# Kernel tuning notes

Hardware: AMD Instinct MI355X
Metric: run time of the kernel (lower is better)

The kernel has to match this reference:

```python
import jax, jax.numpy as jnp
import numpy as np

FORGET_BIAS = 1.0  # tf LSTMCell default

def _lstm_step(c, h, xt, W, b):
    # tf LSTMCell: gates = [x, h] @ W + b, split order (i, j, f, o)
    gates = jnp.concatenate([xt, h], axis=-1) @ W + b
    i, j, f, o = jnp.split(gates, 4, axis=-1)
    c_new = c * jax.nn.sigmoid(f + FORGET_BIAS) + jax.nn.sigmoid(i) * jnp.tanh(j)
    h_new = jnp.tanh(c_new) * jax.nn.sigmoid(o)
    return c_new, h_new

def setup_inputs() -> dict:
    key = jax.random.key(0)
    k1, k2, k3 = jax.random.split(key, 3)
    B, T, H = 512, 1024, 64
    x = jax.random.normal(k1, (B, T, 1), dtype=jnp.float32)
    W1 = jax.random.normal(k2, (1 + H, 4 * H), dtype=jnp.float32) * 0.1
    b1 = jnp.zeros((4 * H,), dtype=jnp.float32)
    W2 = jax.random.normal(k3, (H + 1, 4 * 1), dtype=jnp.float32) * 0.1
    b2 = jnp.zeros((4,), dtype=jnp.float32)
    return {"x": x, "W1": W1, "b1": b1, "W2": W2, "b2": b2}

def reference(x, W1, b1, W2, b2):
    B, T, _ = x.shape
    H = W1.shape[1] // 4
    xs = jnp.swapaxes(x, 0, 1)  # [T, B, 1]

    def step(carry, xt):
        c1, h1, c2, h2 = carry
        c1, h1 = _lstm_step(c1, h1, xt, W1, b1)   # layer 1: in=1, hidden=64
        c2, h2 = _lstm_step(c2, h2, h1, W2, b2)   # layer 2: in=64, hidden=1
        return (c1, h1, c2, h2), h2

    init = (jnp.zeros((B, H), x.dtype), jnp.zeros((B, H), x.dtype),
            jnp.zeros((B, 1), x.dtype), jnp.zeros((B, 1), x.dtype))
    _, ys = jax.lax.scan(step, init, xs)  # ys: [T, B, 1]
    return jnp.swapaxes(ys, 0, 1)  # [B, T, 1]
```

## Files before the change

kernel.cpp:

```cpp
#include <hip/hip_runtime.h>


#define TT 1024

__device__ __forceinline__ float fsig(float x) {
    return __builtin_amdgcn_rcpf(1.f + __expf(-x));
}
__device__ __forceinline__ float ftanh(float x) {
    return 1.f - 2.f * __builtin_amdgcn_rcpf(1.f + __expf(2.f * x));
}

template <int Ctrl, int Rmask>
__device__ __forceinline__ float dpp_add(float x) {
    int t = __builtin_amdgcn_update_dpp(0, __float_as_int(x), Ctrl, Rmask, 0xf, true);
    return x + __int_as_float(t);
}
__device__ __forceinline__ float wave_sum64(float x) {
    x = dpp_add<0x111, 0xf>(x);
    x = dpp_add<0x112, 0xf>(x);
    x = dpp_add<0x114, 0xf>(x);
    x = dpp_add<0x118, 0xf>(x);
    x = dpp_add<0x142, 0xa>(x);
    x = dpp_add<0x143, 0xc>(x);
    return x;
}

__global__ __launch_bounds__(576, 6) void lstm2_kernel(
    const float* __restrict__ x,
    const float* __restrict__ W1,
    const float* __restrict__ b1,
    const float* __restrict__ W2,
    const float* __restrict__ b2,
    float* __restrict__ y)
{
    __shared__ __align__(16) float xs[TT];
    __shared__ __align__(16) float h1s[2][64];
    __shared__ __align__(16) float gs[2][64][4];

    const int tid  = threadIdx.x;
    const int b    = blockIdx.x;
    const int lane = tid & 63;
    const int cw   = tid >> 6;
    const int half = lane >> 5;
    const int l31  = lane & 31;

    if (tid < 256) {
        ((float4*)xs)[tid] = ((const float4*)(x + (size_t)b * TT))[tid];
    }
    if (tid < 128) ((float*)h1s)[tid] = 0.f;

    float* yrow = y + (size_t)b * TT;

    if (cw < 8) {
        const int col   = (cw << 5) | l31;
        const int g     = cw >> 1;
        const int gunit = ((cw & 1) << 5) | l31;

        float w[33];
        float bias = 0.f;
        if (half == 0) {
            w[0] = W1[col];
            bias = b1[col];
#pragma unroll
            for (int j = 1; j <= 32; ++j) w[j] = W1[j * 256 + col];
        } else {
            w[0] = 0.f;
#pragma unroll
            for (int j = 1; j <= 32; ++j) w[j] = W1[(32 + j) * 256 + col];
        }

        const float L2E = 1.4426950408889634f;
        const float mm = (g == 1) ? 2.f * L2E : -L2E;
        const float kk = (g == 2) ? -L2E : 0.f;
        const float aa = (g == 1) ? 1.f : 0.f;
        const float bb = (g == 1) ? -2.f : 1.f;

        const int hrow = half << 3;
        float c1 = 0.f;
        __syncthreads();

#define STEP(PAR, XT) { \
        float a0 = fmaf((XT), w[0], bias), a1 = 0.f, a2 = 0.f, a3 = 0.f; \
        const float4* hb = (const float4*)(&h1s[(PAR) ^ 1][0]); \
        _Pragma("unroll") \
        for (int q = 0; q < 8; ++q) { \
            float4 h4 = hb[hrow + q]; \
            a0 = fmaf(h4.x, w[1 + 4 * q], a0); \
            a1 = fmaf(h4.y, w[2 + 4 * q], a1); \
            a2 = fmaf(h4.z, w[3 + 4 * q], a2); \
            a3 = fmaf(h4.w, w[4 + 4 * q], a3); \
        } \
        float p = (a0 + a1) + (a2 + a3); \
        p += __shfl_xor(p, 32); \
        float act = fmaf(bb, __builtin_amdgcn_rcpf(1.f + exp2f(fmaf(mm, p, kk))), aa); \
        gs[PAR][gunit][g] = act; \
        __syncthreads(); \
        float4 g4 = *(const float4*)(&gs[PAR][lane][0]); \
        c1 = fmaf(c1, g4.z, g4.x * g4.y); \
        float rr = __builtin_amdgcn_rcpf(1.f + exp2f(c1 * (2.f * L2E))); \
        float tt_ = rr * g4.w; \
        h1s[PAR][lane] = fmaf(-2.f, tt_, g4.w); }

        for (int t = 0; t < TT; t += 4) {
            float4 x4 = *(const float4*)(xs + t);
            STEP(0, x4.x)
            STEP(1, x4.y)
            STEP(0, x4.z)
            STEP(1, x4.w)
        }
#undef STEP
        __syncthreads();
    } else {
        float4 w2g4 = *(const float4*)(W2 + lane * 4);
        const float w2h0 = W2[256], w2h1 = W2[257], w2h2 = W2[258], w2h3 = W2[259];
        const float b20 = b2[0], b21 = b2[1], b22 = b2[2], b23 = b2[3];
        float c2 = 0.f, h2 = 0.f;
        __syncthreads();

        for (int t = 0; t < TT; ++t) {
            __syncthreads();
            if (t > 0) {
                const float hv = h1s[(t - 1) & 1][lane];
                const float d0 = wave_sum64(hv * w2g4.x);
                const float d1 = wave_sum64(hv * w2g4.y);
                const float d2 = wave_sum64(hv * w2g4.z);
                const float d3 = wave_sum64(hv * w2g4.w);
                if (lane == 63) {
                    const float i2 = fsig (fmaf(h2, w2h0, d0) + b20);
                    const float j2 = ftanh(fmaf(h2, w2h1, d1) + b21);
                    const float f2 = fsig (fmaf(h2, w2h2, d2) + b22 + 1.f);
                    const float o2 = fsig (fmaf(h2, w2h3, d3) + b23);
                    c2 = fmaf(c2, f2, i2 * j2);
                    h2 = ftanh(c2) * o2;
                    yrow[t - 1] = h2;
                }
            }
        }
        __syncthreads();
        {
            const float hv = h1s[(TT - 1) & 1][lane];
            const float d0 = wave_sum64(hv * w2g4.x);
            const float d1 = wave_sum64(hv * w2g4.y);
            const float d2 = wave_sum64(hv * w2g4.z);
            const float d3 = wave_sum64(hv * w2g4.w);
            if (lane == 63) {
                const float i2 = fsig (fmaf(h2, w2h0, d0) + b20);
                const float j2 = ftanh(fmaf(h2, w2h1, d1) + b21);
                const float f2 = fsig (fmaf(h2, w2h2, d2) + b22 + 1.f);
                const float o2 = fsig (fmaf(h2, w2h3, d3) + b23);
                c2 = fmaf(c2, f2, i2 * j2);
                h2 = ftanh(c2) * o2;
                yrow[TT - 1] = h2;
            }
        }
    }
}

extern "C" void kernel_launch(void* const* d_in, const int* in_sizes, int n_in,
                              void* d_out, int out_size, void* d_ws, size_t ws_size,
                              hipStream_t stream) {
    const float* x  = (const float*)d_in[0];
    const float* W1 = (const float*)d_in[1];
    const float* b1 = (const float*)d_in[2];
    const float* W2 = (const float*)d_in[3];
    const float* b2 = (const float*)d_in[4];
    float* y = (float*)d_out;
    lstm2_kernel<<<512, 576, 0, stream>>>(x, W1, b1, W2, b2, y);
}
```

Before: 696.6 us.

## Process two batch rows per block to share weights and barriers

Each block now handles two sequences. Layer-1 waves compute gate pre-activations for both rows with the same register-resident weights, and two layer-2 waves run one per row. The aim is to halve the block count to one per CU and amortize barrier and latency costs across two independent recurrence chains, adding ILP. The half-wave reduction uses permlane32_swap when available. The cost is more per-step work and register pressure per wave and a larger block.

```diff
diff --git a/kernel.cpp b/kernel.cpp
--- a/kernel.cpp
+++ b/kernel.cpp
@@ -25,7 +25,17 @@
     return x;
 }
 
-__global__ __launch_bounds__(576, 6) void lstm2_kernel(
+#if __has_builtin(__builtin_amdgcn_permlane32_swap)
+__device__ __forceinline__ float halfsum(float p) {
+    auto r = __builtin_amdgcn_permlane32_swap(__float_as_uint(p), __float_as_uint(p),
+                                              false, false);
+    return __uint_as_float(r[0]) + __uint_as_float(r[1]);
+}
+#else
+__device__ __forceinline__ float halfsum(float p) { return p + __shfl_xor(p, 32); }
+#endif
+
+__global__ __launch_bounds__(640, 1) void lstm2_kernel(
     const float* __restrict__ x,
     const float* __restrict__ W1,
     const float* __restrict__ b1,
@@ -33,23 +43,22 @@
     const float* __restrict__ b2,
     float* __restrict__ y)
 {
-    __shared__ __align__(16) float xs[TT];
-    __shared__ __align__(16) float h1s[2][64];
-    __shared__ __align__(16) float gs[2][64][4];
+    __shared__ __align__(16) float xs[2][TT];
+    __shared__ __align__(16) float h1s[2][2][64];
+    __shared__ __align__(16) float gs[2][2][4][64];
 
     const int tid  = threadIdx.x;
-    const int b    = blockIdx.x;
+    const int b0   = blockIdx.x * 2;
     const int lane = tid & 63;
     const int cw   = tid >> 6;
     const int half = lane >> 5;
     const int l31  = lane & 31;
 
-    if (tid < 256) {
-        ((float4*)xs)[tid] = ((const float4*)(x + (size_t)b * TT))[tid];
+    if (tid < 512) {
+        const int e = tid >> 8, i = tid & 255;
+        ((float4*)xs[e])[i] = ((const float4*)(x + (size_t)(b0 + e) * TT))[i];
     }
-    if (tid < 128) ((float*)h1s)[tid] = 0.f;
-
-    float* yrow = y + (size_t)b * TT;
+    if (tid < 256) ((float*)h1s)[tid] = 0.f;
 
     if (cw < 8) {
         const int col   = (cw << 5) | l31;
@@ -76,51 +85,69 @@
         const float bb = (g == 1) ? -2.f : 1.f;
 
         const int hrow = half << 3;
-        float c1 = 0.f;
+        float c1a = 0.f, c1b = 0.f;
         __syncthreads();
 
-#define STEP(PAR, XT) { \
-        float a0 = fmaf((XT), w[0], bias), a1 = 0.f, a2 = 0.f, a3 = 0.f; \
-        const float4* hb = (const float4*)(&h1s[(PAR) ^ 1][0]); \
+#define STEP(PAR, XT0, XT1) { \
+        float a00 = fmaf((XT0), w[0], bias), a01 = 0.f, a02 = 0.f, a03 = 0.f; \
+        float a10 = fmaf((XT1), w[0], bias), a11 = 0.f, a12 = 0.f, a13 = 0.f; \
+        const float4* hb0 = (const float4*)(&h1s[0][(PAR) ^ 1][0]); \
+        const float4* hb1 = (const float4*)(&h1s[1][(PAR) ^ 1][0]); \
         _Pragma("unroll") \
         for (int q = 0; q < 8; ++q) { \
-            float4 h4 = hb[hrow + q]; \
-            a0 = fmaf(h4.x, w[1 + 4 * q], a0); \
-            a1 = fmaf(h4.y, w[2 + 4 * q], a1); \
-            a2 = fmaf(h4.z, w[3 + 4 * q], a2); \
-            a3 = fmaf(h4.w, w[4 + 4 * q], a3); \
+            float4 u0 = hb0[hrow + q]; \
+            float4 u1 = hb1[hrow + q]; \
+            a00 = fmaf(u0.x, w[1 + 4 * q], a00); \
+            a01 = fmaf(u0.y, w[2 + 4 * q], a01); \
+            a02 = fmaf(u0.z, w[3 + 4 * q], a02); \
+            a03 = fmaf(u0.w, w[4 + 4 * q], a03); \
+            a10 = fmaf(u1.x, w[1 + 4 * q], a10); \
+            a11 = fmaf(u1.y, w[2 + 4 * q], a11); \
+            a12 = fmaf(u1.z, w[3 + 4 * q], a12); \
+            a13 = fmaf(u1.w, w[4 + 4 * q], a13); \
         } \
-        float p = (a0 + a1) + (a2 + a3); \
-        p += __shfl_xor(p, 32); \
-        float act = fmaf(bb, __builtin_amdgcn_rcpf(1.f + exp2f(fmaf(mm, p, kk))), aa); \
-        gs[PAR][gunit][g] = act; \
+        float p0 = halfsum((a00 + a01) + (a02 + a03)); \
+        float p1 = halfsum((a10 + a11) + (a12 + a13)); \
+        float act0 = fmaf(bb, __builtin_amdgcn_rcpf(1.f + exp2f(fmaf(mm, p0, kk))), aa); \
+        float act1 = fmaf(bb, __builtin_amdgcn_rcpf(1.f + exp2f(fmaf(mm, p1, kk))), aa); \
+        gs[half][PAR][g][gunit] = half ? act1 : act0; \
         __syncthreads(); \
-        float4 g4 = *(const float4*)(&gs[PAR][lane][0]); \
-        c1 = fmaf(c1, g4.z, g4.x * g4.y); \
-        float rr = __builtin_amdgcn_rcpf(1.f + exp2f(c1 * (2.f * L2E))); \
-        float tt_ = rr * g4.w; \
-        h1s[PAR][lane] = fmaf(-2.f, tt_, g4.w); }
+        { \
+            float i0 = gs[0][PAR][0][lane], j0 = gs[0][PAR][1][lane]; \
+            float f0 = gs[0][PAR][2][lane], o0 = gs[0][PAR][3][lane]; \
+            float i1 = gs[1][PAR][0][lane], j1 = gs[1][PAR][1][lane]; \
+            float f1 = gs[1][PAR][2][lane], o1 = gs[1][PAR][3][lane]; \
+            c1a = fmaf(c1a, f0, i0 * j0); \
+            c1b = fmaf(c1b, f1, i1 * j1); \
+            float r0 = __builtin_amdgcn_rcpf(1.f + exp2f(c1a * (2.f * 1.4426950408889634f))); \
+            float r1 = __builtin_amdgcn_rcpf(1.f + exp2f(c1b * (2.f * 1.4426950408889634f))); \
+            h1s[0][PAR][lane] = fmaf(-2.f, r0 * o0, o0); \
+            h1s[1][PAR][lane] = fmaf(-2.f, r1 * o1, o1); \
+        } }
 
         for (int t = 0; t < TT; t += 4) {
-            float4 x4 = *(const float4*)(xs + t);
-            STEP(0, x4.x)
-            STEP(1, x4.y)
-            STEP(0, x4.z)
-            STEP(1, x4.w)
+            float4 xa = *(const float4*)(xs[0] + t);
+            float4 xb = *(const float4*)(xs[1] + t);
+            STEP(0, xa.x, xb.x)
+            STEP(1, xa.y, xb.y)
+            STEP(0, xa.z, xb.z)
+            STEP(1, xa.w, xb.w)
         }
 #undef STEP
         __syncthreads();
     } else {
+        const int e = cw & 1;
         float4 w2g4 = *(const float4*)(W2 + lane * 4);
         const float w2h0 = W2[256], w2h1 = W2[257], w2h2 = W2[258], w2h3 = W2[259];
         const float b20 = b2[0], b21 = b2[1], b22 = b2[2], b23 = b2[3];
         float c2 = 0.f, h2 = 0.f;
+        float* yrow = y + (size_t)(b0 + e) * TT;
         __syncthreads();
 
         for (int t = 0; t < TT; ++t) {
             __syncthreads();
             if (t > 0) {
-                const float hv = h1s[(t - 1) & 1][lane];
+                const float hv = h1s[e][(t - 1) & 1][lane];
                 const float d0 = wave_sum64(hv * w2g4.x);
                 const float d1 = wave_sum64(hv * w2g4.y);
                 const float d2 = wave_sum64(hv * w2g4.z);
@@ -138,7 +165,7 @@
         }
         __syncthreads();
         {
-            const float hv = h1s[(TT - 1) & 1][lane];
+            const float hv = h1s[e][(TT - 1) & 1][lane];
             const float d0 = wave_sum64(hv * w2g4.x);
             const float d1 = wave_sum64(hv * w2g4.y);
             const float d2 = wave_sum64(hv * w2g4.z);
@@ -165,5 +192,5 @@
     const float* W2 = (const float*)d_in[3];
     const float* b2 = (const float*)d_in[4];
     float* y = (float*)d_out;
-    lstm2_kernel<<<512, 576, 0, stream>>>(x, W1, b1, W2, b2, y);
+    lstm2_kernel<<<256, 640, 0, stream>>>(x, W1, b1, W2, b2, y);
 }
```

After: 706.6 us. No clear change (+1.4%).

## Use one wave per gate with readlane broadcast of h instead of LDS

Applied to the files above, without the earlier changes.

Shrinks the block from 9 waves to 5: each of four compute waves owns one full gate column set (64 weights per lane), so the cross-half shuffle reduction goes away. The hidden state is kept in registers in every wave and broadcast with readlane instead of being read from shared memory. Gates are stored gate-major in LDS, and only wave 0 writes h1 for the layer-2 wave. The cost is 64 serial readlane+FMA steps per timestep rather than 32, plus higher register pressure and lower occupancy bounds.

```diff
diff --git a/kernel.cpp b/kernel.cpp
--- a/kernel.cpp
+++ b/kernel.cpp
@@ -25,7 +25,15 @@
     return x;
 }
 
-__global__ __launch_bounds__(576, 6) void lstm2_kernel(
+__device__ __forceinline__ float bcast(float v, int l) {
+#if __has_builtin(__builtin_amdgcn_readlane)
+    return __uint_as_float(__builtin_amdgcn_readlane(__float_as_uint(v), l));
+#else
+    return __shfl(v, l);
+#endif
+}
+
+__global__ __launch_bounds__(320, 2) void lstm2_kernel(
     const float* __restrict__ x,
     const float* __restrict__ W1,
     const float* __restrict__ b1,
@@ -35,71 +43,59 @@
 {
     __shared__ __align__(16) float xs[TT];
     __shared__ __align__(16) float h1s[2][64];
-    __shared__ __align__(16) float gs[2][64][4];
+    __shared__ __align__(16) float gs[2][4][64];
 
     const int tid  = threadIdx.x;
     const int b    = blockIdx.x;
     const int lane = tid & 63;
     const int cw   = tid >> 6;
-    const int half = lane >> 5;
-    const int l31  = lane & 31;
 
     if (tid < 256) {
         ((float4*)xs)[tid] = ((const float4*)(x + (size_t)b * TT))[tid];
     }
-    if (tid < 128) ((float*)h1s)[tid] = 0.f;
 
     float* yrow = y + (size_t)b * TT;
 
-    if (cw < 8) {
-        const int col   = (cw << 5) | l31;
-        const int g     = cw >> 1;
-        const int gunit = ((cw & 1) << 5) | l31;
+    if (cw < 4) {
+        const int col = (cw << 6) | lane;
 
-        float w[33];
-        float bias = 0.f;
-        if (half == 0) {
-            w[0] = W1[col];
-            bias = b1[col];
+        float w[65];
+        const float bias = b1[col];
+        w[0] = W1[col];
 #pragma unroll
-            for (int j = 1; j <= 32; ++j) w[j] = W1[j * 256 + col];
-        } else {
-            w[0] = 0.f;
-#pragma unroll
-            for (int j = 1; j <= 32; ++j) w[j] = W1[(32 + j) * 256 + col];
-        }
+        for (int j = 1; j <= 64; ++j) w[j] = W1[j * 256 + col];
 
         const float L2E = 1.4426950408889634f;
-        const float mm = (g == 1) ? 2.f * L2E : -L2E;
-        const float kk = (g == 2) ? -L2E : 0.f;
-        const float aa = (g == 1) ? 1.f : 0.f;
-        const float bb = (g == 1) ? -2.f : 1.f;
+        const float mm = (cw == 1) ? 2.f * L2E : -L2E;
+        const float kk = (cw == 2) ? -L2E : 0.f;
+        const float aa = (cw == 1) ? 1.f : 0.f;
+        const float bb = (cw == 1) ? -2.f : 1.f;
 
-        const int hrow = half << 3;
         float c1 = 0.f;
+        float hv = 0.f;
         __syncthreads();
 
 #define STEP(PAR, XT) { \
         float a0 = fmaf((XT), w[0], bias), a1 = 0.f, a2 = 0.f, a3 = 0.f; \
-        const float4* hb = (const float4*)(&h1s[(PAR) ^ 1][0]); \
         _Pragma("unroll") \
-        for (int q = 0; q < 8; ++q) { \
-            float4 h4 = hb[hrow + q]; \
-            a0 = fmaf(h4.x, w[1 + 4 * q], a0); \
-            a1 = fmaf(h4.y, w[2 + 4 * q], a1); \
-            a2 = fmaf(h4.z, w[3 + 4 * q], a2); \
-            a3 = fmaf(h4.w, w[4 + 4 * q], a3); \
+        for (int j = 0; j < 64; j += 4) { \
+            a0 = fmaf(bcast(hv, j + 0), w[j + 1], a0); \
+            a1 = fmaf(bcast(hv, j + 1), w[j + 2], a1); \
+            a2 = fmaf(bcast(hv, j + 2), w[j + 3], a2); \
+            a3 = fmaf(bcast(hv, j + 3), w[j + 4], a3); \
         } \
         float p = (a0 + a1) + (a2 + a3); \
-        p += __shfl_xor(p, 32); \
         float act = fmaf(bb, __builtin_amdgcn_rcpf(1.f + exp2f(fmaf(mm, p, kk))), aa); \
-        gs[PAR][gunit][g] = act; \
+        gs[PAR][cw][lane] = act; \
         __syncthreads(); \
-        float4 g4 = *(const float4*)(&gs[PAR][lane][0]); \
-        c1 = fmaf(c1, g4.z, g4.x * g4.y); \
-        float rr = __builtin_amdgcn_rcpf(1.f + exp2f(c1 * (2.f * L2E))); \
-        float tt_ = rr * g4.w; \
-        h1s[PAR][lane] = fmaf(-2.f, tt_, g4.w); }
+        { \
+            float i_ = gs[PAR][0][lane], j_ = gs[PAR][1][lane]; \
+            float f_ = gs[PAR][2][lane], o_ = gs[PAR][3][lane]; \
+            c1 = fmaf(c1, f_, i_ * j_); \
+            float rr = __builtin_amdgcn_rcpf(1.f + exp2f(c1 * (2.f * 1.4426950408889634f))); \
+            hv = fmaf(-2.f, rr * o_, o_); \
+            if (cw == 0) h1s[PAR][lane] = hv; \
+        } }
 
         for (int t = 0; t < TT; t += 4) {
             float4 x4 = *(const float4*)(xs + t);
@@ -165,5 +161,5 @@
     const float* W2 = (const float*)d_in[3];
     const float* b2 = (const float*)d_in[4];
     float* y = (float*)d_out;
-    lstm2_kernel<<<512, 576, 0, stream>>>(x, W1, b1, W2, b2, y);
+    lstm2_kernel<<<512, 320, 0, stream>>>(x, W1, b1, W2, b2, y);
 }
```

Result: slower. 874.9 us (+25.6%).
